# Kernel tuning notes

Measured on AMD Instinct MI355X. Metric: run time of the kernel, lower is better.

Reference implementation:

```python
import jax, jax.numpy as jnp
import numpy as np

HEADS = 16


def setup_inputs() -> dict:
    key = jax.random.key(0)
    ks = jax.random.split(key, 7)
    B, N, MEM, DIM = 2, 2048, 2048, 1024
    J = MEM + N
    x = jax.random.normal(ks[0], (B, N, DIM), dtype=jnp.float32)
    mem = jax.random.normal(ks[1], (B, MEM, DIM), dtype=jnp.float32)
    expire_mask = jax.random.uniform(ks[2], (B, 1, 1, J), dtype=jnp.float32)
    Wq = jax.random.normal(ks[3], (DIM, DIM), dtype=jnp.float32) * 0.02
    Wkv = jax.random.normal(ks[4], (DIM, 2 * DIM), dtype=jnp.float32) * 0.02
    Wo = jax.random.normal(ks[5], (DIM, DIM), dtype=jnp.float32) * 0.02
    bo = jnp.zeros((DIM,), dtype=jnp.float32)
    return {"x": x, "mem": mem, "expire_mask": expire_mask,
            "Wq": Wq, "Wkv": Wkv, "Wo": Wo, "bo": bo}


def reference(x, mem, expire_mask, Wq, Wkv, Wo, bo):
    b, n, dim = x.shape
    h = HEADS
    d = dim // h
    scale = d ** -0.5
    mem_len = mem.shape[1]

    q = x @ Wq                                   # [b, n, dim]
    context = jnp.concatenate([mem, x], axis=1)  # [b, j, dim]
    kv = context @ Wkv                           # [b, j, 2*dim]
    k, v = jnp.split(kv, 2, axis=-1)

    def to_heads(t):
        bb, nn, _ = t.shape
        return t.reshape(bb, nn, h, d).transpose(0, 2, 1, 3)  # b h n d

    q, k, v = map(to_heads, (q, k, v))

    dots = jnp.einsum('bhid,bhjd->bhij', q, k) * scale  # [b,h,n,j]
    j_len = dots.shape[-1]
    # causal mask with memory offset: position i attends to j <= i + mem_len
    i_idx = jnp.arange(n)[:, None]
    j_idx = jnp.arange(j_len)[None, :]
    causal = j_idx > (i_idx + mem_len)           # True => masked
    dots = jnp.where(causal[None, None], -jnp.inf, dots)

    attn = jax.nn.softmax(dots, axis=-1)
    attn = attn * expire_mask                    # post-softmax expire gating

    out = jnp.einsum('bhij,bhjd->bhid', attn, v)  # [b,h,n,d]
    out = out.transpose(0, 2, 1, 3).reshape(b, n, dim)
    return out @ Wo + bo
```

## Files before the change

kernel.cpp:

```cpp
#include <hip/hip_runtime.h>
#include <cstdint>

typedef __bf16 bf16_t;
typedef __attribute__((ext_vector_type(2))) __bf16 bf16x2;
typedef __attribute__((ext_vector_type(4))) __bf16 bf16x4;
typedef __attribute__((ext_vector_type(8))) __bf16 bf16x8;
typedef __attribute__((ext_vector_type(4))) float f32x4;
typedef __attribute__((ext_vector_type(16))) float f32x16;
typedef __attribute__((ext_vector_type(4))) int i32x4;

constexpr int Bx = 2, Nx = 2048, MEMx = 2048, Jx = 4096, DIMx = 1024, Hx = 16, HDx = 64;

__device__ __forceinline__ void gload_lds16(const bf16_t* g, bf16_t* lds) {
  __builtin_amdgcn_global_load_lds(
      (const __attribute__((address_space(1))) unsigned int*)g,
      (__attribute__((address_space(3))) unsigned int*)lds, 16, 0, 0);
}

__device__ __forceinline__ int pk2(float a, float b) {
  bf16x2 t;
  t[0] = (bf16_t)a;
  t[1] = (bf16_t)b;
  return __builtin_bit_cast(int, t);
}

__device__ __forceinline__ void pl32swap(int& a, int& b) {
  asm volatile("v_permlane32_swap_b32 %0, %1" : "+v"(a), "+v"(b));
}

__device__ __forceinline__ float fmax3(float a, float b, float c) {
  float d;
  asm("v_max3_f32 %0, %1, %2, %3" : "=v"(d) : "v"(a), "v"(b), "v"(c));
  return d;
}

__global__ void k_build8(const float* __restrict__ x, const float* __restrict__ mem,
                         bf16_t* __restrict__ xb, bf16_t* __restrict__ ctxb) {
  const int XT8 = (Bx * Nx * DIMx) >> 3;
  const int CT8 = (Bx * Jx * DIMx) >> 3;
  for (int i = blockIdx.x * blockDim.x + threadIdx.x; i < XT8 + CT8;
       i += gridDim.x * blockDim.x) {
    const float* src;
    bf16_t* dst;
    if (i < XT8) {
      src = x + ((int64_t)i << 3);
      dst = xb + ((int64_t)i << 3);
    } else {
      int64_t c = (int64_t)(i - XT8) << 3;
      int bb = (int)(c >> 22);
      int rr = (int)(c & ((1 << 22) - 1));
      int j = rr >> 10, d = rr & 1023;
      src = (j < MEMx) ? mem + (((int64_t)(bb * MEMx + j)) << 10) + d
                       : x + (((int64_t)(bb * Nx + (j - MEMx))) << 10) + d;
      dst = ctxb + c;
    }
    float4 a = *(const float4*)src;
    float4 b = *(const float4*)(src + 4);
    bf16x8 v;
    v[0] = (bf16_t)a.x; v[1] = (bf16_t)a.y; v[2] = (bf16_t)a.z; v[3] = (bf16_t)a.w;
    v[4] = (bf16_t)b.x; v[5] = (bf16_t)b.y; v[6] = (bf16_t)b.z; v[7] = (bf16_t)b.w;
    *(bf16x8*)dst = v;
  }
}

__global__ void k_transpose_tiled(const float* __restrict__ W, bf16_t* __restrict__ WT,
                                  int K, int Nc) {
  __shared__ bf16_t t[32][33];
  const int tx = threadIdx.x & 31, ty = threadIdx.x >> 5;
  const int n0 = blockIdx.x * 32, k0 = blockIdx.y * 32;
#pragma unroll
  for (int r = 0; r < 4; ++r)
    t[ty + 8 * r][tx] = (bf16_t)W[(int64_t)(k0 + ty + 8 * r) * Nc + n0 + tx];
  __syncthreads();
#pragma unroll
  for (int r = 0; r < 4; ++r)
    WT[(int64_t)(n0 + ty + 8 * r) * K + k0 + tx] = t[tx][ty + 8 * r];
}

template <int MODE>
__launch_bounds__(256)
__global__ void k_gemm_bt(const bf16_t* __restrict__ A, const bf16_t* __restrict__ BT,
                          void* __restrict__ Cv, const float* __restrict__ bias,
                          const float* __restrict__ gate, bf16_t* __restrict__ VT,
                          float scale, int M, int Nc, int K) {
  __shared__ bf16_t As[2][128 * 32];
  __shared__ bf16_t Bs[2][128 * 32];
  const int tid = threadIdx.x;
  const int w = tid >> 6, l = tid & 63;
  const int lr = l & 15, lg = l >> 4;
  const int m0 = blockIdx.y * 128, n0 = blockIdx.x * 128;
  const int wm = (w >> 1) * 64, wn = (w & 1) * 64;

  const int srow = w * 16 + (l >> 2);
  const int scol = (l & 3) * 8;
  const bf16_t* ga0 = A + (int64_t)(m0 + srow) * K + scol;
  const bf16_t* gb0 = BT + (int64_t)(n0 + srow) * K + scol;

  auto stage = [&](int bufi, int k0) {
    bf16_t* lA = &As[bufi][0] + w * 512;
    bf16_t* lB = &Bs[bufi][0] + w * 512;
    gload_lds16(ga0 + k0, lA);
    gload_lds16(ga0 + (int64_t)64 * K + k0, lA + 2048);
    gload_lds16(gb0 + k0, lB);
    gload_lds16(gb0 + (int64_t)64 * K + k0, lB + 2048);
  };

  f32x4 acc[4][4] = {};

  const int nsteps = K >> 5;
  stage(0, 0);
  stage(1, 32);

  for (int t = 0; t < nsteps; ++t) {
    const int cur = t & 1;
    if (t + 1 < nsteps)
      asm volatile("s_waitcnt vmcnt(4)" ::: "memory");
    else
      asm volatile("s_waitcnt vmcnt(0)" ::: "memory");
    __builtin_amdgcn_s_barrier();
    __builtin_amdgcn_sched_barrier(0);

    bf16x8 af[4], bfr[4];
#pragma unroll
    for (int q = 0; q < 4; ++q)
      af[q] = *(const bf16x8*)(&As[cur][0] + (wm + q * 16 + lr) * 32 + lg * 8);
#pragma unroll
    for (int q = 0; q < 4; ++q)
      bfr[q] = *(const bf16x8*)(&Bs[cur][0] + (wn + q * 16 + lr) * 32 + lg * 8);
#pragma unroll
    for (int mt = 0; mt < 4; ++mt)
#pragma unroll
      for (int nt = 0; nt < 4; ++nt)
        acc[mt][nt] = __builtin_amdgcn_mfma_f32_16x16x32_bf16(af[mt], bfr[nt],
                                                              acc[mt][nt], 0, 0, 0);
    __builtin_amdgcn_s_barrier();
    __builtin_amdgcn_sched_barrier(0);
    if (t + 2 < nsteps) stage(cur, (t + 2) << 5);
  }

#pragma unroll
  for (int mt = 0; mt < 4; ++mt) {
#pragma unroll
    for (int nt = 0; nt < 4; ++nt) {
      int col = n0 + wn + nt * 16 + lr;
      int row0 = m0 + wm + mt * 16 + lg * 4;
      if constexpr (MODE == 0) {
#pragma unroll
        for (int r = 0; r < 4; ++r)
          ((bf16_t*)Cv)[(int64_t)(row0 + r) * Nc + col] =
              (bf16_t)(acc[mt][nt][r] * scale);
      } else if constexpr (MODE == 1) {
#pragma unroll
        for (int r = 0; r < 4; ++r)
          ((float*)Cv)[(int64_t)(row0 + r) * Nc + col] = acc[mt][nt][r] + bias[col];
      } else {
        if (col < 1024) {
#pragma unroll
          for (int r = 0; r < 4; ++r)
            ((bf16_t*)Cv)[(int64_t)(row0 + r) * 1024 + col] = (bf16_t)acc[mt][nt][r];
        } else {
          int hh = (col - 1024) >> 6, dd = col & 63;
          int bb = row0 >> 12, jj = row0 & (Jx - 1);
          bf16x4 ov;
#pragma unroll
          for (int r = 0; r < 4; ++r)
            ov[r] = (bf16_t)(acc[mt][nt][r] * gate[row0 + r]);
          *(bf16x4*)(VT + (((int64_t)(bb * Hx + hh) * HDx + dd) << 12) + jj) = ov;
        }
      }
    }
  }
}

__launch_bounds__(256)
__global__ void k_attn(const bf16_t* __restrict__ Q, const bf16_t* __restrict__ Kbuf,
                       const bf16_t* __restrict__ VT, bf16_t* __restrict__ Opart,
                       float2* __restrict__ ML) {
  __shared__ bf16_t Ks[2][64 * 64];
  __shared__ bf16_t Vs[2][64 * 64];

  const int tid = threadIdx.x;
  const int w = tid >> 6, l = tid & 63;
  const int ql = l & 31, hi = l >> 5;

  const int lin = blockIdx.x;
  const int qi0 = lin & 15, h = (lin >> 4) & 15;
  const int c = (lin >> 8) & 1, b = lin >> 9;
  const int qi = b ? (15 - qi0) : qi0;
  const int q0 = qi * 128;

  const bf16_t* Qb = Q + ((int64_t)b * Nx) * DIMx + h * HDx;
  const bf16_t* Kb = Kbuf + ((int64_t)b * Jx) * 1024 + h * HDx;
  const bf16_t* Vb = VT + ((int64_t)(b * Hx + h) * HDx << 12);

  const int qrow = q0 + w * 32 + ql;

  bf16x8 qf[4];
#pragma unroll
  for (int dt = 0; dt < 4; ++dt)
    qf[dt] = *(const bf16x8*)(Qb + (int64_t)qrow * DIMx + dt * 16 + hi * 8);
  asm volatile("s_waitcnt vmcnt(0)" ::: "memory");

  int koff[2][4], voff[2][4];
#pragma unroll
  for (int jb = 0; jb < 2; ++jb)
#pragma unroll
    for (int dt = 0; dt < 4; ++dt)
      koff[jb][dt] = (jb * 32 + ql) * 128 + (((dt * 2 + hi) * 16) ^ ((ql & 7) * 16));
#pragma unroll
  for (int db = 0; db < 2; ++db)
#pragma unroll
    for (int jt = 0; jt < 4; ++jt)
      voff[db][jt] = (db * 32 + ql) * 128 + (((jt * 2 + hi) * 16) ^ ((ql & 7) * 16));

  bf16x8 onesv;
#pragma unroll
  for (int i = 0; i < 8; ++i) onesv[i] = (bf16_t)1.0f;

  f32x16 o[2] = {};
  f32x16 ol = {};
  float mrun = 8.0f;

  const int srow8 = l >> 3;
  const int swcol = ((l & 7) ^ srow8) * 8;
  const int jend_full = (Jx < q0 + 128 + MEMx) ? Jx : (q0 + 128 + MEMx);
  const int T = jend_full >> 6;
  const int half = T >> 1;
  const int jstart = c ? (half << 6) : 0;
  const int nt_tiles = c ? (T - half) : half;
  const f32x16 z16 = {};

  const bf16_t* ksrc0 = Kb + (int64_t)(w * 16 + srow8) * 1024 + swcol;
  const bf16_t* vsrc0 = Vb + (int64_t)(w * 16 + srow8) * Jx + swcol;

  auto stage = [&](int bufi, int j0) {
    bf16_t* kd = &Ks[bufi][0] + w * 1024;
    const bf16_t* ks = ksrc0 + (int64_t)j0 * 1024;
    gload_lds16(ks, kd);
    gload_lds16(ks + 8 * 1024, kd + 512);
    bf16_t* vd = &Vs[bufi][0] + w * 1024;
    const bf16_t* vs = vsrc0 + j0;
    gload_lds16(vs, vd);
    gload_lds16(vs + 8 * Jx, vd + 512);
  };

  stage(0, jstart);
  stage(1, jstart + 64);

  for (int t = 0; t < nt_tiles; ++t) {
    const int cur = t & 1;
    const int j0 = jstart + (t << 6);
    if (t + 1 < nt_tiles)
      asm volatile("s_waitcnt vmcnt(4)" ::: "memory");
    else
      asm volatile("s_waitcnt vmcnt(0)" ::: "memory");
    __builtin_amdgcn_s_barrier();
    __builtin_amdgcn_sched_barrier(0);

    const char* KsC = (const char*)&Ks[cur][0];
    const char* VsC = (const char*)&Vs[cur][0];

    f32x16 s[2];
    __builtin_amdgcn_s_setprio(1);
#pragma unroll
    for (int jb = 0; jb < 2; ++jb) {
      f32x16 acc = z16;
#pragma unroll
      for (int dt = 0; dt < 4; ++dt) {
        bf16x8 kf = *(const bf16x8*)(KsC + koff[jb][dt]);
        acc = __builtin_amdgcn_mfma_f32_32x32x16_bf16(kf, qf[dt], acc, 0, 0, 0);
      }
      s[jb] = acc;
    }
    __builtin_amdgcn_s_setprio(0);

    if (j0 + 63 > q0 + MEMx) {
#pragma unroll
      for (int jb = 0; jb < 2; ++jb)
#pragma unroll
        for (int r = 0; r < 16; ++r) {
          int j = j0 + jb * 32 + (r & 3) + (r >> 2) * 8 + hi * 4;
          if (j > qrow + MEMx) s[jb][r] = -1e30f;
        }
    }

    float t12[12];
#pragma unroll
    for (int i = 0; i < 10; ++i)
      t12[i] = fmax3(s[(3 * i) >> 4][(3 * i) & 15], s[(3 * i + 1) >> 4][(3 * i + 1) & 15],
                     s[(3 * i + 2) >> 4][(3 * i + 2) & 15]);
    t12[10] = s[1][14];
    t12[11] = s[1][15];
    float t4[4];
#pragma unroll
    for (int i = 0; i < 4; ++i) t4[i] = fmax3(t12[3 * i], t12[3 * i + 1], t12[3 * i + 2]);
    float tm = fmaxf(fmax3(t4[0], t4[1], t4[2]), t4[3]);
    tm = fmaxf(tm, __shfl_xor(tm, 32));

    if (!__all(tm <= mrun + 8.f)) {
      float mnew = fmaxf(mrun, tm);
      float al = exp2f(mrun - mnew);
      mrun = mnew;
#pragma unroll
      for (int r = 0; r < 16; ++r) ol[r] *= al;
#pragma unroll
      for (int db = 0; db < 2; ++db)
#pragma unroll
        for (int r = 0; r < 16; ++r) o[db][r] *= al;
    }

#pragma unroll
    for (int jb = 0; jb < 2; ++jb)
#pragma unroll
      for (int r = 0; r < 16; ++r) s[jb][r] = exp2f(s[jb][r] - mrun);

    bf16x8 pfrag[4];
#pragma unroll
    for (int jb = 0; jb < 2; ++jb) {
      int pw[8];
#pragma unroll
      for (int g = 0; g < 8; ++g) pw[g] = pk2(s[jb][2 * g], s[jb][2 * g + 1]);
      pl32swap(pw[0], pw[2]);
      pl32swap(pw[1], pw[3]);
      pl32swap(pw[4], pw[6]);
      pl32swap(pw[5], pw[7]);
      i32x4 f0 = {pw[0], pw[1], pw[2], pw[3]};
      i32x4 f1 = {pw[4], pw[5], pw[6], pw[7]};
      pfrag[jb * 2] = __builtin_bit_cast(bf16x8, f0);
      pfrag[jb * 2 + 1] = __builtin_bit_cast(bf16x8, f1);
    }

    __builtin_amdgcn_s_setprio(1);
#pragma unroll
    for (int jt = 0; jt < 4; ++jt) {
      bf16x8 vf0 = *(const bf16x8*)(VsC + voff[0][jt]);
      o[0] = __builtin_amdgcn_mfma_f32_32x32x16_bf16(vf0, pfrag[jt], o[0], 0, 0, 0);
      bf16x8 vf1 = *(const bf16x8*)(VsC + voff[1][jt]);
      o[1] = __builtin_amdgcn_mfma_f32_32x32x16_bf16(vf1, pfrag[jt], o[1], 0, 0, 0);
      ol = __builtin_amdgcn_mfma_f32_32x32x16_bf16(onesv, pfrag[jt], ol, 0, 0, 0);
    }
    __builtin_amdgcn_s_setprio(0);

    __builtin_amdgcn_s_barrier();
    __builtin_amdgcn_sched_barrier(0);
    if (t + 2 < nt_tiles) stage(cur, jstart + ((t + 2) << 6));
  }

  bf16_t* op = Opart + (int64_t)c * (Bx * Nx * DIMx) +
               (int64_t)(b * Nx + qrow) * DIMx + h * HDx;
#pragma unroll
  for (int db = 0; db < 2; ++db)
#pragma unroll
    for (int g = 0; g < 4; ++g) {
      bf16x4 ov;
#pragma unroll
      for (int r = 0; r < 4; ++r) ov[r] = (bf16_t)o[db][g * 4 + r];
      *(bf16x4*)(op + db * 32 + g * 8 + hi * 4) = ov;
    }
  if (hi == 0)
    ML[((int64_t)(c * Bx + b) * Hx + h) * Nx + qrow] = make_float2(mrun, ol[0]);
}

__global__ void k_combine(const bf16_t* __restrict__ Op, const float2* __restrict__ ML,
                          bf16_t* __restrict__ Ho) {
  const int64_t CH = (int64_t)Bx * Nx * DIMx;
  int i = blockIdx.x * blockDim.x + threadIdx.x;
  const int total = (int)(CH >> 3);
  if (i >= total) return;
  int64_t off = (int64_t)i * 8;
  int bqh = (int)(off >> 6);
  int h = bqh & 15;
  int bq = bqh >> 4;
  int b = bq >> 11, q = bq & (Nx - 1);
  float2 ml0 = ML[((int64_t)b * Hx + h) * Nx + q];
  float2 ml1 = ML[((int64_t)(Bx + b) * Hx + h) * Nx + q];
  float M = fmaxf(ml0.x, ml1.x);
  float a0 = exp2f(ml0.x - M), a1 = exp2f(ml1.x - M);
  float inv = 1.f / (a0 * ml0.y + a1 * ml1.y);
  a0 *= inv;
  a1 *= inv;
  bf16x8 v0 = *(const bf16x8*)(Op + off);
  bf16x8 v1 = *(const bf16x8*)(Op + CH + off);
  bf16x8 outv;
#pragma unroll
  for (int r = 0; r < 8; ++r)
    outv[r] = (bf16_t)(a0 * (float)v0[r] + a1 * (float)v1[r]);
  *(bf16x8*)(Ho + off) = outv;
}

extern "C" void kernel_launch(void* const* d_in, const int* in_sizes, int n_in,
                              void* d_out, int out_size, void* d_ws, size_t ws_size,
                              hipStream_t stream) {
  const float* x    = (const float*)d_in[0];
  const float* mem  = (const float*)d_in[1];
  const float* expm = (const float*)d_in[2];
  const float* Wq   = (const float*)d_in[3];
  const float* Wkv  = (const float*)d_in[4];
  const float* Wo   = (const float*)d_in[5];
  const float* bo   = (const float*)d_in[6];
  float* out = (float*)d_out;

  bf16_t* p = (bf16_t*)d_ws;
  bf16_t* xb   = p; p += (size_t)Bx * Nx * DIMx;
  bf16_t* ctxb = p; p += (size_t)Bx * Jx * DIMx;
  bf16_t* WqT  = p; p += (size_t)DIMx * DIMx;
  bf16_t* WkvT = p; p += (size_t)DIMx * 2 * DIMx;
  bf16_t* WoT  = p; p += (size_t)DIMx * DIMx;
  bf16_t* Qb   = p; p += (size_t)Bx * Nx * DIMx;
  bf16_t* KVb  = p; p += (size_t)Bx * Jx * 2 * DIMx;
  bf16_t* Ho   = p; p += (size_t)Bx * Nx * DIMx;

  bf16_t* Kbuf = KVb;
  bf16_t* VT   = KVb + (size_t)Bx * Jx * 1024;
  bf16_t* Opart = ctxb;
  float2* ML    = (float2*)xb;

  k_build8<<<2048, 256, 0, stream>>>(x, mem, xb, ctxb);
  k_transpose_tiled<<<dim3(32, 32), 256, 0, stream>>>(Wq, WqT, DIMx, DIMx);
  k_transpose_tiled<<<dim3(64, 32), 256, 0, stream>>>(Wkv, WkvT, DIMx, 2 * DIMx);
  k_transpose_tiled<<<dim3(32, 32), 256, 0, stream>>>(Wo, WoT, DIMx, DIMx);

  const float qscale = 0.125f * 1.4426950408889634f;
  k_gemm_bt<0><<<dim3(1024 / 128, 4096 / 128), 256, 0, stream>>>(
      xb, WqT, Qb, nullptr, nullptr, nullptr, qscale, Bx * Nx, DIMx, DIMx);
  k_gemm_bt<2><<<dim3(2048 / 128, 8192 / 128), 256, 0, stream>>>(
      ctxb, WkvT, Kbuf, nullptr, expm, VT, 1.0f, Bx * Jx, 2 * DIMx, DIMx);

  k_attn<<<1024, 256, 0, stream>>>(Qb, Kbuf, VT, Opart, ML);
  k_combine<<<(Bx * Nx * DIMx / 8 + 255) / 256, 256, 0, stream>>>(Opart, ML, Ho);

  k_gemm_bt<1><<<dim3(1024 / 128, 4096 / 128), 256, 0, stream>>>(
      Ho, WoT, out, bo, nullptr, nullptr, 1.0f, Bx * Nx, DIMx, DIMx);
}
```

Baseline: 254.3 us.

## Load K fragments straight into registers and split KV range at the memory boundary

K tiles are no longer staged through LDS. Each lane reads its K MFMA fragments directly from global memory into registers, one tile ahead, while V keeps the double-buffered global-to-LDS path with adjusted vmcnt waits. The two key-range chunks are also redefined: chunk 0 covers the memory keys and chunk 1 covers the causal keys of x, instead of an even half split. This halves the LDS footprint and drops the LDS reads for K. In exchange, global-load latency for K is exposed with only one-tile lookahead, and chunk-1 blocks now have uneven tile counts, which can hurt load balance.

```diff
diff --git a/kernel.cpp b/kernel.cpp
--- a/kernel.cpp
+++ b/kernel.cpp
@@ -176,7 +176,6 @@
 __global__ void k_attn(const bf16_t* __restrict__ Q, const bf16_t* __restrict__ Kbuf,
                        const bf16_t* __restrict__ VT, bf16_t* __restrict__ Opart,
                        float2* __restrict__ ML) {
-  __shared__ bf16_t Ks[2][64 * 64];
   __shared__ bf16_t Vs[2][64 * 64];
 
   const int tid = threadIdx.x;
@@ -201,12 +200,7 @@
     qf[dt] = *(const bf16x8*)(Qb + (int64_t)qrow * DIMx + dt * 16 + hi * 8);
   asm volatile("s_waitcnt vmcnt(0)" ::: "memory");
 
-  int koff[2][4], voff[2][4];
-#pragma unroll
-  for (int jb = 0; jb < 2; ++jb)
-#pragma unroll
-    for (int dt = 0; dt < 4; ++dt)
-      koff[jb][dt] = (jb * 32 + ql) * 128 + (((dt * 2 + hi) * 16) ^ ((ql & 7) * 16));
+  int voff[2][4];
 #pragma unroll
   for (int db = 0; db < 2; ++db)
 #pragma unroll
@@ -223,41 +217,42 @@
 
   const int srow8 = l >> 3;
   const int swcol = ((l & 7) ^ srow8) * 8;
-  const int jend_full = (Jx < q0 + 128 + MEMx) ? Jx : (q0 + 128 + MEMx);
-  const int T = jend_full >> 6;
-  const int half = T >> 1;
-  const int jstart = c ? (half << 6) : 0;
-  const int nt_tiles = c ? (T - half) : half;
+  const int jstart = c * 2048;
+  const int jend = c ? ((Jx < q0 + 128 + MEMx) ? Jx : (q0 + 128 + MEMx)) : 2048;
+  const int nt_tiles = (jend - jstart) >> 6;
   const f32x16 z16 = {};
 
-  const bf16_t* ksrc0 = Kb + (int64_t)(w * 16 + srow8) * 1024 + swcol;
   const bf16_t* vsrc0 = Vb + (int64_t)(w * 16 + srow8) * Jx + swcol;
 
-  auto stage = [&](int bufi, int j0) {
-    bf16_t* kd = &Ks[bufi][0] + w * 1024;
-    const bf16_t* ks = ksrc0 + (int64_t)j0 * 1024;
-    gload_lds16(ks, kd);
-    gload_lds16(ks + 8 * 1024, kd + 512);
+  auto stageV = [&](int bufi, int j0) {
     bf16_t* vd = &Vs[bufi][0] + w * 1024;
     const bf16_t* vs = vsrc0 + j0;
     gload_lds16(vs, vd);
     gload_lds16(vs + 8 * Jx, vd + 512);
   };
 
-  stage(0, jstart);
-  stage(1, jstart + 64);
+  const bf16_t* kp0 = Kb + (int64_t)(jstart + ql) * 1024 + hi * 8;
+  const bf16_t* kp1 = kp0 + 32 * 1024;
+
+  bf16x8 kf[2][4];
+  stageV(0, jstart);
+  stageV(1, jstart + 64);
+#pragma unroll
+  for (int dt = 0; dt < 4; ++dt) {
+    kf[0][dt] = *(const bf16x8*)(kp0 + dt * 16);
+    kf[1][dt] = *(const bf16x8*)(kp1 + dt * 16);
+  }
 
   for (int t = 0; t < nt_tiles; ++t) {
     const int cur = t & 1;
     const int j0 = jstart + (t << 6);
     if (t + 1 < nt_tiles)
-      asm volatile("s_waitcnt vmcnt(4)" ::: "memory");
+      asm volatile("s_waitcnt vmcnt(2)" ::: "memory");
     else
       asm volatile("s_waitcnt vmcnt(0)" ::: "memory");
     __builtin_amdgcn_s_barrier();
     __builtin_amdgcn_sched_barrier(0);
 
-    const char* KsC = (const char*)&Ks[cur][0];
     const char* VsC = (const char*)&Vs[cur][0];
 
     f32x16 s[2];
@@ -266,13 +261,21 @@
     for (int jb = 0; jb < 2; ++jb) {
       f32x16 acc = z16;
 #pragma unroll
+      for (int dt = 0; dt < 4; ++dt)
+        acc = __builtin_amdgcn_mfma_f32_32x32x16_bf16(kf[jb][dt], qf[dt], acc, 0, 0, 0);
+      s[jb] = acc;
+    }
+    __builtin_amdgcn_s_setprio(0);
+
+    if (t + 1 < nt_tiles) {
+      kp0 += 64 * 1024;
+      kp1 += 64 * 1024;
+#pragma unroll
       for (int dt = 0; dt < 4; ++dt) {
-        bf16x8 kf = *(const bf16x8*)(KsC + koff[jb][dt]);
-        acc = __builtin_amdgcn_mfma_f32_32x32x16_bf16(kf, qf[dt], acc, 0, 0, 0);
+        kf[0][dt] = *(const bf16x8*)(kp0 + dt * 16);
+        kf[1][dt] = *(const bf16x8*)(kp1 + dt * 16);
       }
-      s[jb] = acc;
-    }
-    __builtin_amdgcn_s_setprio(0);
+    }
 
     if (j0 + 63 > q0 + MEMx) {
 #pragma unroll
@@ -343,7 +346,7 @@
 
     __builtin_amdgcn_s_barrier();
     __builtin_amdgcn_sched_barrier(0);
-    if (t + 2 < nt_tiles) stage(cur, jstart + ((t + 2) << 6));
+    if (t + 2 < nt_tiles) stageV(cur, jstart + ((t + 2) << 6));
   }
 
   bf16_t* op = Opart + (int64_t)c * (Bx * Nx * DIMx) +
```

New measurement: 280.4 us. 10.3% more time.

## Software-pipeline QK of next tile with triple-buffered K/V in attention

Applied to the files above, without the earlier changes.

The attention loop now computes QK^T scores for the next key tile before doing softmax and PV on the current one. K/V staging moves from double to triple buffering so the next two tiles can load while the current tile is consumed, and the loop is unrolled by two with alternating score registers. The key-range split also changes: one block half takes the full memory segment and the other takes the causal segment. The aim is to hide score-MFMA and load latency behind the softmax math. The new split can leave the two halves unevenly loaded, and the extra score registers plus the occupancy hint of 2 may cause register spills.

```diff
diff --git a/kernel.cpp b/kernel.cpp
--- a/kernel.cpp
+++ b/kernel.cpp
@@ -172,12 +172,12 @@
   }
 }
 
-__launch_bounds__(256)
+__launch_bounds__(256, 2)
 __global__ void k_attn(const bf16_t* __restrict__ Q, const bf16_t* __restrict__ Kbuf,
                        const bf16_t* __restrict__ VT, bf16_t* __restrict__ Opart,
                        float2* __restrict__ ML) {
-  __shared__ bf16_t Ks[2][64 * 64];
-  __shared__ bf16_t Vs[2][64 * 64];
+  __shared__ bf16_t Ks[3][64 * 64];
+  __shared__ bf16_t Vs[3][64 * 64];
 
   const int tid = threadIdx.x;
   const int w = tid >> 6, l = tid & 63;
@@ -223,128 +223,136 @@
 
   const int srow8 = l >> 3;
   const int swcol = ((l & 7) ^ srow8) * 8;
-  const int jend_full = (Jx < q0 + 128 + MEMx) ? Jx : (q0 + 128 + MEMx);
-  const int T = jend_full >> 6;
-  const int half = T >> 1;
-  const int jstart = c ? (half << 6) : 0;
-  const int nt_tiles = c ? (T - half) : half;
+  const int jstart = c * 2048;
+  const int jend = c ? ((Jx < q0 + 128 + MEMx) ? Jx : (q0 + 128 + MEMx)) : 2048;
+  const int nt_tiles = (jend - jstart) >> 6;
   const f32x16 z16 = {};
 
   const bf16_t* ksrc0 = Kb + (int64_t)(w * 16 + srow8) * 1024 + swcol;
   const bf16_t* vsrc0 = Vb + (int64_t)(w * 16 + srow8) * Jx + swcol;
-
-  auto stage = [&](int bufi, int j0) {
-    bf16_t* kd = &Ks[bufi][0] + w * 1024;
+  const char* KsBase = (const char*)&Ks[0][0];
+  const char* VsBase = (const char*)&Vs[0][0];
+
+  auto stageKV = [&](int bi, int j0) {
+    bf16_t* kd = &Ks[bi][0] + w * 1024;
     const bf16_t* ks = ksrc0 + (int64_t)j0 * 1024;
     gload_lds16(ks, kd);
     gload_lds16(ks + 8 * 1024, kd + 512);
-    bf16_t* vd = &Vs[bufi][0] + w * 1024;
+    bf16_t* vd = &Vs[bi][0] + w * 1024;
     const bf16_t* vs = vsrc0 + j0;
     gload_lds16(vs, vd);
     gload_lds16(vs + 8 * Jx, vd + 512);
   };
 
-  stage(0, jstart);
-  stage(1, jstart + 64);
-
-  for (int t = 0; t < nt_tiles; ++t) {
-    const int cur = t & 1;
-    const int j0 = jstart + (t << 6);
-    if (t + 1 < nt_tiles)
-      asm volatile("s_waitcnt vmcnt(4)" ::: "memory");
-    else
-      asm volatile("s_waitcnt vmcnt(0)" ::: "memory");
-    __builtin_amdgcn_s_barrier();
-    __builtin_amdgcn_sched_barrier(0);
-
-    const char* KsC = (const char*)&Ks[cur][0];
-    const char* VsC = (const char*)&Vs[cur][0];
-
-    f32x16 s[2];
+  f32x16 sA[2], sB[2];
+  int ib = 0, inb = 1, ist = 2;
+
+  stageKV(0, jstart);
+  stageKV(1, jstart + 64);
+  asm volatile("s_waitcnt vmcnt(6)" ::: "memory");
+  __builtin_amdgcn_s_barrier();
+  __builtin_amdgcn_sched_barrier(0);
+  {
     __builtin_amdgcn_s_setprio(1);
 #pragma unroll
     for (int jb = 0; jb < 2; ++jb) {
       f32x16 acc = z16;
 #pragma unroll
       for (int dt = 0; dt < 4; ++dt) {
-        bf16x8 kf = *(const bf16x8*)(KsC + koff[jb][dt]);
+        bf16x8 kf = *(const bf16x8*)(KsBase + koff[jb][dt]);
         acc = __builtin_amdgcn_mfma_f32_32x32x16_bf16(kf, qf[dt], acc, 0, 0, 0);
       }
-      s[jb] = acc;
+      sA[jb] = acc;
     }
     __builtin_amdgcn_s_setprio(0);
-
-    if (j0 + 63 > q0 + MEMx) {
-#pragma unroll
-      for (int jb = 0; jb < 2; ++jb)
-#pragma unroll
-        for (int r = 0; r < 16; ++r) {
-          int j = j0 + jb * 32 + (r & 3) + (r >> 2) * 8 + hi * 4;
-          if (j > qrow + MEMx) s[jb][r] = -1e30f;
-        }
-    }
-
-    float t12[12];
-#pragma unroll
-    for (int i = 0; i < 10; ++i)
-      t12[i] = fmax3(s[(3 * i) >> 4][(3 * i) & 15], s[(3 * i + 1) >> 4][(3 * i + 1) & 15],
-                     s[(3 * i + 2) >> 4][(3 * i + 2) & 15]);
-    t12[10] = s[1][14];
-    t12[11] = s[1][15];
-    float t4[4];
-#pragma unroll
-    for (int i = 0; i < 4; ++i) t4[i] = fmax3(t12[3 * i], t12[3 * i + 1], t12[3 * i + 2]);
-    float tm = fmaxf(fmax3(t4[0], t4[1], t4[2]), t4[3]);
-    tm = fmaxf(tm, __shfl_xor(tm, 32));
-
-    if (!__all(tm <= mrun + 8.f)) {
-      float mnew = fmaxf(mrun, tm);
-      float al = exp2f(mrun - mnew);
-      mrun = mnew;
-#pragma unroll
-      for (int r = 0; r < 16; ++r) ol[r] *= al;
-#pragma unroll
-      for (int db = 0; db < 2; ++db)
-#pragma unroll
-        for (int r = 0; r < 16; ++r) o[db][r] *= al;
-    }
-
-#pragma unroll
-    for (int jb = 0; jb < 2; ++jb)
-#pragma unroll
-      for (int r = 0; r < 16; ++r) s[jb][r] = exp2f(s[jb][r] - mrun);
-
-    bf16x8 pfrag[4];
-#pragma unroll
-    for (int jb = 0; jb < 2; ++jb) {
-      int pw[8];
-#pragma unroll
-      for (int g = 0; g < 8; ++g) pw[g] = pk2(s[jb][2 * g], s[jb][2 * g + 1]);
-      pl32swap(pw[0], pw[2]);
-      pl32swap(pw[1], pw[3]);
-      pl32swap(pw[4], pw[6]);
-      pl32swap(pw[5], pw[7]);
-      i32x4 f0 = {pw[0], pw[1], pw[2], pw[3]};
-      i32x4 f1 = {pw[4], pw[5], pw[6], pw[7]};
-      pfrag[jb * 2] = __builtin_bit_cast(bf16x8, f0);
-      pfrag[jb * 2 + 1] = __builtin_bit_cast(bf16x8, f1);
-    }
-
-    __builtin_amdgcn_s_setprio(1);
-#pragma unroll
-    for (int jt = 0; jt < 4; ++jt) {
-      bf16x8 vf0 = *(const bf16x8*)(VsC + voff[0][jt]);
-      o[0] = __builtin_amdgcn_mfma_f32_32x32x16_bf16(vf0, pfrag[jt], o[0], 0, 0, 0);
-      bf16x8 vf1 = *(const bf16x8*)(VsC + voff[1][jt]);
-      o[1] = __builtin_amdgcn_mfma_f32_32x32x16_bf16(vf1, pfrag[jt], o[1], 0, 0, 0);
-      ol = __builtin_amdgcn_mfma_f32_32x32x16_bf16(onesv, pfrag[jt], ol, 0, 0, 0);
-    }
-    __builtin_amdgcn_s_setprio(0);
-
-    __builtin_amdgcn_s_barrier();
-    __builtin_amdgcn_sched_barrier(0);
-    if (t + 2 < nt_tiles) stage(cur, jstart + ((t + 2) << 6));
   }
+
+#define ATTN_BODY(SCUR, SNXT, T)                                                     \
+  do {                                                                               \
+    const int j0_ = jstart + ((T) << 6);                                             \
+    if ((T) + 1 < nt_tiles)                                                          \
+      asm volatile("s_waitcnt vmcnt(2)" ::: "memory");                               \
+    else                                                                             \
+      asm volatile("s_waitcnt vmcnt(0)" ::: "memory");                               \
+    __builtin_amdgcn_s_barrier();                                                    \
+    __builtin_amdgcn_sched_barrier(0);                                               \
+    if ((T) + 2 < nt_tiles) stageKV(ist, jstart + (((T) + 2) << 6));                 \
+    if ((T) + 1 < nt_tiles) {                                                        \
+      const char* Kn_ = KsBase + inb * 8192;                                         \
+      __builtin_amdgcn_s_setprio(1);                                                 \
+      _Pragma("unroll") for (int jb = 0; jb < 2; ++jb) {                             \
+        f32x16 acc_ = z16;                                                           \
+        _Pragma("unroll") for (int dt = 0; dt < 4; ++dt) {                           \
+          bf16x8 kf_ = *(const bf16x8*)(Kn_ + koff[jb][dt]);                         \
+          acc_ = __builtin_amdgcn_mfma_f32_32x32x16_bf16(kf_, qf[dt], acc_, 0, 0, 0);\
+        }                                                                            \
+        SNXT[jb] = acc_;                                                             \
+      }                                                                              \
+      __builtin_amdgcn_s_setprio(0);                                                 \
+      __builtin_amdgcn_sched_barrier(0);                                             \
+    }                                                                                \
+    if (j0_ + 63 > q0 + MEMx) {                                                      \
+      _Pragma("unroll") for (int jb = 0; jb < 2; ++jb)                               \
+      _Pragma("unroll") for (int r = 0; r < 16; ++r) {                               \
+        int j_ = j0_ + jb * 32 + (r & 3) + (r >> 2) * 8 + hi * 4;                    \
+        if (j_ > qrow + MEMx) SCUR[jb][r] = -1e30f;                                  \
+      }                                                                              \
+    }                                                                                \
+    float t12_[12];                                                                  \
+    _Pragma("unroll") for (int i = 0; i < 10; ++i)                                   \
+        t12_[i] = fmax3(SCUR[(3 * i) >> 4][(3 * i) & 15],                            \
+                        SCUR[(3 * i + 1) >> 4][(3 * i + 1) & 15],                    \
+                        SCUR[(3 * i + 2) >> 4][(3 * i + 2) & 15]);                   \
+    t12_[10] = SCUR[1][14];                                                          \
+    t12_[11] = SCUR[1][15];                                                          \
+    float t4_[4];                                                                    \
+    _Pragma("unroll") for (int i = 0; i < 4; ++i)                                    \
+        t4_[i] = fmax3(t12_[3 * i], t12_[3 * i + 1], t12_[3 * i + 2]);               \
+    float tm_ = fmaxf(fmax3(t4_[0], t4_[1], t4_[2]), t4_[3]);                        \
+    tm_ = fmaxf(tm_, __shfl_xor(tm_, 32));                                           \
+    if (!__all(tm_ <= mrun + 8.f)) {                                                 \
+      float mnew_ = fmaxf(mrun, tm_);                                                \
+      float al_ = exp2f(mrun - mnew_);                                               \
+      mrun = mnew_;                                                                  \
+      _Pragma("unroll") for (int r = 0; r < 16; ++r) ol[r] *= al_;                   \
+      _Pragma("unroll") for (int db = 0; db < 2; ++db)                               \
+      _Pragma("unroll") for (int r = 0; r < 16; ++r) o[db][r] *= al_;                \
+    }                                                                                \
+    _Pragma("unroll") for (int jb = 0; jb < 2; ++jb)                                 \
+    _Pragma("unroll") for (int r = 0; r < 16; ++r)                                   \
+        SCUR[jb][r] = exp2f(SCUR[jb][r] - mrun);                                     \
+    bf16x8 pfrag_[4];                                                                \
+    _Pragma("unroll") for (int jb = 0; jb < 2; ++jb) {                               \
+      int pw_[8];                                                                    \
+      _Pragma("unroll") for (int g = 0; g < 8; ++g)                                  \
+          pw_[g] = pk2(SCUR[jb][2 * g], SCUR[jb][2 * g + 1]);                        \
+      pl32swap(pw_[0], pw_[2]);                                                      \
+      pl32swap(pw_[1], pw_[3]);                                                      \
+      pl32swap(pw_[4], pw_[6]);                                                      \
+      pl32swap(pw_[5], pw_[7]);                                                      \
+      i32x4 f0_ = {pw_[0], pw_[1], pw_[2], pw_[3]};                                  \
+      i32x4 f1_ = {pw_[4], pw_[5], pw_[6], pw_[7]};                                  \
+      pfrag_[jb * 2] = __builtin_bit_cast(bf16x8, f0_);                              \
+      pfrag_[jb * 2 + 1] = __builtin_bit_cast(bf16x8, f1_);                          \
+    }                                                                                \
+    const char* Vc_ = VsBase + ib * 8192;                                            \
+    __builtin_amdgcn_s_setprio(1);                                                   \
+    _Pragma("unroll") for (int jt = 0; jt < 4; ++jt) {                               \
+      bf16x8 vf0_ = *(const bf16x8*)(Vc_ + voff[0][jt]);                             \
+      o[0] = __builtin_amdgcn_mfma_f32_32x32x16_bf16(vf0_, pfrag_[jt], o[0], 0, 0, 0);\
+      bf16x8 vf1_ = *(const bf16x8*)(Vc_ + voff[1][jt]);                             \
+      o[1] = __builtin_amdgcn_mfma_f32_32x32x16_bf16(vf1_, pfrag_[jt], o[1], 0, 0, 0);\
+      ol = __builtin_amdgcn_mfma_f32_32x32x16_bf16(onesv, pfrag_[jt], ol, 0, 0, 0);  \
+    }                                                                                \
+    __builtin_amdgcn_s_setprio(0);                                                   \
+    int tmp_ = ib; ib = inb; inb = ist; ist = tmp_;                                  \
+  } while (0)
+
+  for (int t = 0; t < nt_tiles; t += 2) {
+    ATTN_BODY(sA, sB, t);
+    ATTN_BODY(sB, sA, t + 1);
+  }
+#undef ATTN_BODY
 
   bf16_t* op = Opart + (int64_t)c * (Bx * Nx * DIMx) +
                (int64_t)(b * Nx + qrow) * DIMx + h * HDx;
```

Measured after the change: 248.0 us (median of 5 runs). 2.5% less time.
